# Kernel tuning notes

Hardware: AMD Instinct MI355X
Metric: run time of the kernel (lower is better)

## Reference

```python
import jax, jax.numpy as jnp
import numpy as np
import math

FACTOR = 5  # ProbAttention factor; scale=None -> 1/sqrt(D); mask_flag=True; output_attention=False


def setup_inputs() -> dict:
    key = jax.random.key(0)
    k1, k2, k3, k4 = jax.random.split(key, 4)
    B, L, H, D = 4, 2048, 8, 64
    sample_k = FACTOR * int(np.ceil(np.log(L)))  # 40
    queries = jax.random.normal(k1, (B, L, H, D), dtype=jnp.float32)
    keys = jax.random.normal(k2, (B, L, H, D), dtype=jnp.float32)
    values = jax.random.normal(k3, (B, L, H, D), dtype=jnp.float32)
    index_sample = jax.random.randint(k4, (L, sample_k), 0, L, dtype=jnp.int32)
    attn_mask = jnp.zeros((1,), dtype=bool)  # unused: ProbMask is rebuilt internally
    return {"queries": queries, "keys": keys, "values": values,
            "index_sample": index_sample, "attn_mask": attn_mask}


def reference(queries, keys, values, index_sample, attn_mask):
    B, L_Q, H, D = queries.shape
    L_K = keys.shape[1]
    # [B, L, H, D] -> [B, H, L, D]
    Q = jnp.transpose(queries, (0, 2, 1, 3))
    K = jnp.transpose(keys, (0, 2, 1, 3))
    V = jnp.transpose(values, (0, 2, 1, 3))

    U_part = max(1, min(FACTOR * int(math.ceil(math.log(L_K))), L_K))  # sample_k
    u = max(1, min(FACTOR * int(math.ceil(math.log(L_Q))), L_Q))       # n_top
    sample_k = U_part  # == index_sample.shape[1]

    # --- _prob_QK: sampled scores -> sparsity measure M -> top-u queries ---
    K_sample = K[:, :, index_sample, :]                       # [B,H,L_Q,sample_k,D]
    Q_K_sample = jnp.einsum('bhqd,bhqsd->bhqs', Q, K_sample)  # [B,H,L_Q,sample_k]
    M = Q_K_sample.max(axis=-1) - Q_K_sample.sum(axis=-1) / sample_k
    M_top = jax.lax.top_k(M, u)[1]                            # [B,H,u]

    Q_reduce = jnp.take_along_axis(Q, M_top[..., None], axis=2)   # [B,H,u,D]
    scale = 1.0 / math.sqrt(D)
    scores = jnp.einsum('bhud,bhkd->bhuk', Q_reduce, K) * scale   # [B,H,u,L_K]

    # --- initial context (mask_flag=True, L_Q == L_V): cumulative sum of V ---
    context = jnp.cumsum(V, axis=2)                               # [B,H,L_Q,D]

    # --- ProbMask: causal mask rows gathered at selected query positions ---
    causal = jnp.triu(jnp.ones((L_Q, L_K), dtype=bool), 1)
    mask = causal[M_top]                                          # [B,H,u,L_K]
    scores = jnp.where(mask, -jnp.inf, scores)

    attn = jax.nn.softmax(scores, axis=-1)
    upd = jnp.einsum('bhuk,bhkd->bhud', attn, V)                  # [B,H,u,D]

    b_idx = jnp.arange(B)[:, None, None]
    h_idx = jnp.arange(H)[None, :, None]
    context = context.at[b_idx, h_idx, M_top].set(upd)

    return jnp.transpose(context, (0, 2, 1, 3))  # [B,L_Q,H,D]
```

## Files before the change

kernel.cpp:

```cpp
#include <hip/hip_runtime.h>
#include <hip/hip_bf16.h>
#include <hip/hip_fp16.h>
#include <cstdint>

#define BB 4
#define LL 2048
#define HH 8
#define DD 64
#define SK 40
#define UU 40
#define LDK 68
#define NSEG32 64
#define NSEG64 32
#define PSTRIDE 34

__global__ __launch_bounds__(256) void k_sample_score(
    const float* __restrict__ Q, const float* __restrict__ K,
    const int* __restrict__ idxs, float* __restrict__ M) {
  int j = blockIdx.x;
  int xcd = j & 7, r = j >> 3;
  int bh = (xcd << 2) | (r >> 6);
  int qc = r & 63;
  int b = bh >> 3, h = bh & 7;
  int t = threadIdx.x;
  int ql = t >> 3, sp = t & 7;
  int q = qc * 32 + ql;

  __shared__ int sidx[SK][32];
  for (int i = t; i < SK * 32; i += 256)
    sidx[i >> 5][i & 31] = idxs[(qc * 32 + (i & 31)) * SK + (i >> 5)];
  __syncthreads();

  const float* qrow = Q + ((size_t)((b * LL + q) * HH + h)) * DD;
  float4 qa = *reinterpret_cast<const float4*>(qrow + sp * 4);
  float4 qb = *reinterpret_cast<const float4*>(qrow + 32 + sp * 4);

  const float* kb = K + (size_t)b * (LL * HH * DD) + h * DD;
  float mx = -1e30f, sm = 0.f;
#pragma unroll 4
  for (int s = 0; s < SK; s++) {
    int ks = sidx[s][ql];
    const float* kr = kb + (size_t)ks * (HH * DD);
    float4 ca = *reinterpret_cast<const float4*>(kr + sp * 4);
    float4 cb = *reinterpret_cast<const float4*>(kr + 32 + sp * 4);
    float dot = qa.x * ca.x + qa.y * ca.y + qa.z * ca.z + qa.w * ca.w +
                qb.x * cb.x + qb.y * cb.y + qb.z * cb.z + qb.w * cb.w;
    dot += __shfl_xor(dot, 1);
    dot += __shfl_xor(dot, 2);
    dot += __shfl_xor(dot, 4);
    mx = fmaxf(mx, dot);
    sm += dot;
  }
  if (sp == 0) M[bh * LL + q] = mx - sm * (1.0f / SK);
}

__global__ __launch_bounds__(256) void k_topk(const float* __restrict__ M,
                                              int* __restrict__ Mtop) {
  int bh = blockIdx.x;
  int t = threadIdx.x;
  __shared__ unsigned long long sk[LL];
  for (int i = t; i < LL; i += 256) {
    unsigned u = __float_as_uint(M[bh * LL + i]);
    u = (u & 0x80000000u) ? ~u : (u | 0x80000000u);
    sk[i] = ((unsigned long long)u << 32) | (unsigned)(~i);
  }
  __syncthreads();
  for (int k = 2; k <= LL; k <<= 1) {
    for (int j = k >> 1; j > 0; j >>= 1) {
#pragma unroll
      for (int m = 0; m < LL / 512; m++) {
        int p = t + m * 256;
        int i = ((p & ~(j - 1)) << 1) | (p & (j - 1));
        int l = i | j;
        unsigned long long a = sk[i], c = sk[l];
        bool asc = (i & k) == 0;
        if ((a > c) == asc) { sk[i] = c; sk[l] = a; }
      }
      __syncthreads();
    }
  }
  if (t < UU) {
    int e = (int)(~(unsigned)sk[LL - 1 - t]) & (LL - 1);
    Mtop[bh * UU + t] = e;
  }
}

__global__ __launch_bounds__(64) void k_chunksum16(const float* __restrict__ V,
                                                   float* __restrict__ CS16) {
  int j = blockIdx.x;
  int xcd = j & 7, r = j >> 3;
  int bh = (xcd << 2) | (r >> 7);
  int c = r & 127;
  int b = bh >> 3, h = bh & 7;
  int t = threadIdx.x, d4 = t & 15, r4 = t >> 4;
  const float4* vp = reinterpret_cast<const float4*>(
      V + ((size_t)((b * LL + c * 16 + r4 * 4) * HH + h)) * DD) + d4;
  float4 v0 = vp[0], v1 = vp[128], v2 = vp[256], v3 = vp[384];
  float4 s;
  s.x = v0.x + v1.x + v2.x + v3.x;
  s.y = v0.y + v1.y + v2.y + v3.y;
  s.z = v0.z + v1.z + v2.z + v3.z;
  s.w = v0.w + v1.w + v2.w + v3.w;
#pragma unroll
  for (int sh = 16; sh < 64; sh <<= 1) {
    s.x += __shfl_xor(s.x, sh);
    s.y += __shfl_xor(s.y, sh);
    s.z += __shfl_xor(s.z, sh);
    s.w += __shfl_xor(s.w, sh);
  }
  if (r4 == 0)
    *reinterpret_cast<float4*>(CS16 + ((size_t)bh * 128 + c) * 64 + d4 * 4) = s;
}

__global__ __launch_bounds__(256) void k_prefix16(const float* __restrict__ CS16,
                                                  float* __restrict__ PS16) {
  int bh = blockIdx.x;
  int t = threadIdx.x, w = t >> 6, d = t & 63;
  float cs[32];
  const float* base = CS16 + ((size_t)bh * 128 + w * 32) * 64 + d;
#pragma unroll
  for (int cc = 0; cc < 32; cc++) cs[cc] = base[cc * 64];
  float tot = 0.f;
#pragma unroll
  for (int cc = 0; cc < 32; cc++) tot += cs[cc];
  __shared__ float totw[4][64];
  totw[w][d] = tot;
  __syncthreads();
  float run = 0.f;
#pragma unroll
  for (int w2 = 0; w2 < 4; w2++)
    if (w2 < w) run += totw[w2][d];
  float* pbase = PS16 + ((size_t)bh * 128 + w * 32) * 64 + d;
#pragma unroll
  for (int cc = 0; cc < 32; cc++) { pbase[cc * 64] = run; run += cs[cc]; }
}

__global__ __launch_bounds__(64) void k_cumsum16(const float* __restrict__ V,
                                                 const float* __restrict__ PS16,
                                                 float* __restrict__ Out) {
  int j = blockIdx.x;
  int xcd = j & 7, r = j >> 3;
  int bh = (xcd << 2) | (r >> 7);
  int c = r & 127;
  int b = bh >> 3, h = bh & 7;
  int t = threadIdx.x, d4 = t & 15, r4 = t >> 4;
  size_t rowbase = ((size_t)((b * LL + c * 16 + r4 * 4) * HH + h)) * DD;
  const float4* vp = reinterpret_cast<const float4*>(V + rowbase) + d4;
  float4 v0 = vp[0], v1 = vp[128], v2 = vp[256], v3 = vp[384];
  float4 i0 = v0;
  float4 i1 = {i0.x + v1.x, i0.y + v1.y, i0.z + v1.z, i0.w + v1.w};
  float4 i2 = {i1.x + v2.x, i1.y + v2.y, i1.z + v2.z, i1.w + v2.w};
  float4 i3 = {i2.x + v3.x, i2.y + v3.y, i2.z + v3.z, i2.w + v3.w};
  float4 incl = i3;
  float4 u1;
  u1.x = __shfl_up(incl.x, 16); u1.y = __shfl_up(incl.y, 16);
  u1.z = __shfl_up(incl.z, 16); u1.w = __shfl_up(incl.w, 16);
  if (r4 >= 1) { incl.x += u1.x; incl.y += u1.y; incl.z += u1.z; incl.w += u1.w; }
  float4 u2;
  u2.x = __shfl_up(incl.x, 32); u2.y = __shfl_up(incl.y, 32);
  u2.z = __shfl_up(incl.z, 32); u2.w = __shfl_up(incl.w, 32);
  if (r4 >= 2) { incl.x += u2.x; incl.y += u2.y; incl.z += u2.z; incl.w += u2.w; }
  float4 ex = {incl.x - i3.x, incl.y - i3.y, incl.z - i3.z, incl.w - i3.w};
  float4 ps = *reinterpret_cast<const float4*>(
      PS16 + ((size_t)bh * 128 + c) * 64 + d4 * 4);
  float4 base4 = {ps.x + ex.x, ps.y + ex.y, ps.z + ex.z, ps.w + ex.w};
  float4* op = reinterpret_cast<float4*>(Out + rowbase) + d4;
  float4 o;
  o = {base4.x + i0.x, base4.y + i0.y, base4.z + i0.z, base4.w + i0.w}; op[0]   = o;
  o = {base4.x + i1.x, base4.y + i1.y, base4.z + i1.z, base4.w + i1.w}; op[128] = o;
  o = {base4.x + i2.x, base4.y + i2.y, base4.z + i2.z, base4.w + i2.w}; op[256] = o;
  o = {base4.x + i3.x, base4.y + i3.y, base4.z + i3.z, base4.w + i3.w}; op[384] = o;
}

__global__ __launch_bounds__(256) void k_attn_part32(
    const float* __restrict__ Q, const float* __restrict__ K,
    const float* __restrict__ V, const int* __restrict__ Mtop,
    float* __restrict__ Part) {
  int j = blockIdx.x;
  int xcd = j & 7, r_ = j >> 3;
  int bh = (xcd << 2) | (r_ & 3);
  int seg = r_ >> 2;
  int b = bh >> 3, h = bh & 7;
  int s0 = seg * 32;

  int t = threadIdx.x;
  int w = t >> 6, lane = t & 63;
  int kk = lane & 15, gg = lane >> 4;

  __shared__ float Kt[32 * LDK];
  __shared__ float psh[4][32];
  __shared__ int midx[UU];

  if (t < UU) midx[t] = Mtop[bh * UU + t];

  const float4* kg = reinterpret_cast<const float4*>(
      K + ((size_t)((b * LL + s0) * HH + h)) * DD);
#pragma unroll
  for (int i = 0; i < 2; i++) {
    int f = t + i * 256;
    int r = f >> 4, col = f & 15;
    float4 kv4 = kg[(size_t)r * (HH * DD / 4) + col];
    *reinterpret_cast<float4*>(&Kt[r * LDK + col * 4]) = kv4;
  }

  const float* vgp = V + ((size_t)((b * LL + s0) * HH + h)) * DD + lane;
  float vreg[32];
#pragma unroll
  for (int k = 0; k < 32; k++) vreg[k] = vgp[(size_t)k * (HH * DD)];

  __syncthreads();

  for (int uu = 0; uu < 10; uu++) {
    int u = w + uu * 4;
    int idx = midx[u];
    if (idx < s0) continue;
    int kend = idx - s0;
    if (kend > 31) kend = 31;

    const float4* qv = reinterpret_cast<const float4*>(
        Q + ((size_t)((b * LL + idx) * HH + h)) * DD + gg * 16);
    float4 qr0 = qv[0], qr1 = qv[1], qr2 = qv[2], qr3 = qv[3];

    float s0v, s1v;
    {
      const float4* kr = reinterpret_cast<const float4*>(&Kt[kk * LDK + gg * 16]);
      float4 c0 = kr[0], c1 = kr[1], c2 = kr[2], c3 = kr[3];
      float dp = qr0.x * c0.x + qr0.y * c0.y + qr0.z * c0.z + qr0.w * c0.w +
                 qr1.x * c1.x + qr1.y * c1.y + qr1.z * c1.z + qr1.w * c1.w +
                 qr2.x * c2.x + qr2.y * c2.y + qr2.z * c2.z + qr2.w * c2.w +
                 qr3.x * c3.x + qr3.y * c3.y + qr3.z * c3.z + qr3.w * c3.w;
      dp += __shfl_xor(dp, 16);
      dp += __shfl_xor(dp, 32);
      s0v = (kk <= kend) ? dp * 0.125f : -1e30f;
    }
    {
      const float4* kr = reinterpret_cast<const float4*>(&Kt[(16 + kk) * LDK + gg * 16]);
      float4 c0 = kr[0], c1 = kr[1], c2 = kr[2], c3 = kr[3];
      float dp = qr0.x * c0.x + qr0.y * c0.y + qr0.z * c0.z + qr0.w * c0.w +
                 qr1.x * c1.x + qr1.y * c1.y + qr1.z * c1.z + qr1.w * c1.w +
                 qr2.x * c2.x + qr2.y * c2.y + qr2.z * c2.z + qr2.w * c2.w +
                 qr3.x * c3.x + qr3.y * c3.y + qr3.z * c3.z + qr3.w * c3.w;
      dp += __shfl_xor(dp, 16);
      dp += __shfl_xor(dp, 32);
      s1v = (16 + kk <= kend) ? dp * 0.125f : -1e30f;
    }

    float m = fmaxf(s0v, s1v);
    m = fmaxf(m, __shfl_xor(m, 1));
    m = fmaxf(m, __shfl_xor(m, 2));
    m = fmaxf(m, __shfl_xor(m, 4));
    m = fmaxf(m, __shfl_xor(m, 8));
    float p0 = (kk <= kend) ? __expf(s0v - m) : 0.f;
    float p1 = (16 + kk <= kend) ? __expf(s1v - m) : 0.f;
    float l = p0 + p1;
    l += __shfl_xor(l, 1);
    l += __shfl_xor(l, 2);
    l += __shfl_xor(l, 4);
    l += __shfl_xor(l, 8);

    if (gg == 0) { psh[w][kk] = p0; psh[w][16 + kk] = p1; }

    float acc = 0.f;
#pragma unroll
    for (int kq = 0; kq < 8; kq++) {
      float4 pp = *reinterpret_cast<const float4*>(&psh[w][kq * 4]);
      acc += pp.x * vreg[kq * 4 + 0] + pp.y * vreg[kq * 4 + 1] +
             pp.z * vreg[kq * 4 + 2] + pp.w * vreg[kq * 4 + 3];
    }

    float* pb = Part + ((size_t)(bh * UU + u) * NSEG32 + seg) * PSTRIDE;
    __half* ph = reinterpret_cast<__half*>(pb + 2);
    ph[lane] = __float2half(acc);
    if (lane == 0) { pb[0] = m; pb[1] = l; }
  }
}

__global__ __launch_bounds__(256) void k_attn_part64(
    const float* __restrict__ Q, const float* __restrict__ K,
    const float* __restrict__ V, const int* __restrict__ Mtop,
    float* __restrict__ Part) {
  int j = blockIdx.x;
  int xcd = j & 7, r_ = j >> 3;
  int bh = (xcd << 2) | (r_ & 3);
  int seg = r_ >> 2;
  int b = bh >> 3, h = bh & 7;
  int s0 = seg * 64;

  int t = threadIdx.x;
  int w = t >> 6, lane = t & 63;
  int kk = lane & 15, gg = lane >> 4;

  __shared__ float Kt[64 * LDK];
  __shared__ float Vt[64 * LDK];
  __shared__ int midx[UU];

  if (t < UU) midx[t] = Mtop[bh * UU + t];

  const float4* kg = reinterpret_cast<const float4*>(
      K + ((size_t)((b * LL + s0) * HH + h)) * DD);
  const float4* vg = reinterpret_cast<const float4*>(
      V + ((size_t)((b * LL + s0) * HH + h)) * DD);
#pragma unroll
  for (int i = 0; i < 4; i++) {
    int f = t + i * 256;
    int r = f >> 4, col = f & 15;
    float4 kv4 = kg[(size_t)r * (HH * DD / 4) + col];
    float4 vv4 = vg[(size_t)r * (HH * DD / 4) + col];
    *reinterpret_cast<float4*>(&Kt[r * LDK + col * 4]) = kv4;
    *reinterpret_cast<float4*>(&Vt[r * LDK + col * 4]) = vv4;
  }
  __syncthreads();

  for (int uu = 0; uu < 10; uu++) {
    int u = w + uu * 4;
    int idx = midx[u];
    if (idx < s0) continue;
    int kend = idx - s0;
    if (kend > 63) kend = 63;

    const float4* qv = reinterpret_cast<const float4*>(
        Q + ((size_t)((b * LL + idx) * HH + h)) * DD + gg * 16);
    float4 qr0 = qv[0], qr1 = qv[1], qr2 = qv[2], qr3 = qv[3];

    float m = -1e30f, l = 0.f, acc = 0.f;
#pragma unroll
    for (int ks = 0; ks < 4; ks++) {
      if (ks * 16 > kend) break;
      int row = ks * 16 + kk;
      float dp = 0.f;
      const float4* kr = reinterpret_cast<const float4*>(&Kt[row * LDK + gg * 16]);
      float4 c0 = kr[0], c1 = kr[1], c2 = kr[2], c3 = kr[3];
      dp += qr0.x * c0.x + qr0.y * c0.y + qr0.z * c0.z + qr0.w * c0.w;
      dp += qr1.x * c1.x + qr1.y * c1.y + qr1.z * c1.z + qr1.w * c1.w;
      dp += qr2.x * c2.x + qr2.y * c2.y + qr2.z * c2.z + qr2.w * c2.w;
      dp += qr3.x * c3.x + qr3.y * c3.y + qr3.z * c3.z + qr3.w * c3.w;
      dp += __shfl_xor(dp, 16);
      dp += __shfl_xor(dp, 32);
      bool valid = (row <= kend);
      float s = valid ? dp * 0.125f : -1e30f;
      float cm = s;
      cm = fmaxf(cm, __shfl_xor(cm, 1));
      cm = fmaxf(cm, __shfl_xor(cm, 2));
      cm = fmaxf(cm, __shfl_xor(cm, 4));
      cm = fmaxf(cm, __shfl_xor(cm, 8));
      float mn = fmaxf(m, cm);
      float f_ = __expf(m - mn);
      float p = valid ? __expf(s - mn) : 0.f;
      float ps = p;
      ps += __shfl_xor(ps, 1);
      ps += __shfl_xor(ps, 2);
      ps += __shfl_xor(ps, 4);
      ps += __shfl_xor(ps, 8);
      l = l * f_ + ps;
      m = mn;
      acc *= f_;
#pragma unroll
      for (int k2 = 0; k2 < 16; k2++) {
        float pk = __shfl(p, k2);
        acc += pk * Vt[(ks * 16 + k2) * LDK + lane];
      }
    }

    float* pb = Part + ((size_t)(bh * UU + u) * NSEG64 + seg) * PSTRIDE;
    __half* ph = reinterpret_cast<__half*>(pb + 2);
    ph[lane] = __float2half(acc);
    if (lane == 0) { pb[0] = m; pb[1] = l; }
  }
}

__global__ __launch_bounds__(64) void k_attn_merge(
    const int* __restrict__ Mtop, const float* __restrict__ Part,
    float* __restrict__ Out, int shift, int nsegmax) {
  int blk = blockIdx.x;
  int bh = blk / UU, u = blk % UU;
  int b = bh >> 3, h = bh & 7;
  int lane = threadIdx.x;
  int idx = Mtop[bh * UU + u];
  int nseg = (idx >> shift) + 1;

  const float* base = Part + (size_t)(bh * UU + u) * nsegmax * PSTRIDE;
  float ms = -1e30f, ls = 0.f;
  if (lane < nseg) { ms = base[lane * PSTRIDE]; ls = base[lane * PSTRIDE + 1]; }
  float M0 = ms;
#pragma unroll
  for (int s = 1; s < 64; s <<= 1) M0 = fmaxf(M0, __shfl_xor(M0, s));
  float e = (lane < nseg) ? __expf(ms - M0) : 0.f;
  float lt = ls * e;
#pragma unroll
  for (int s = 1; s < 64; s <<= 1) lt += __shfl_xor(lt, s);

  __shared__ float ew[64];
  ew[lane] = e;
  __syncthreads();

  float A = 0.f;
  for (int s = 0; s < nseg; s++) {
    const __half* ha = reinterpret_cast<const __half*>(base + s * PSTRIDE + 2);
    A += ew[s] * __half2float(ha[lane]);
  }
  Out[((size_t)((b * LL + idx) * HH + h)) * DD + lane] = A / lt;
}

__global__ __launch_bounds__(256) void k_attn_fused(
    const float* __restrict__ Q, const float* __restrict__ K,
    const float* __restrict__ V, const int* __restrict__ Mtop,
    float* __restrict__ Out) {
  int j = blockIdx.x;
  int xcd = j & 7, slot = j >> 3;
  int bh = (xcd << 2) | (slot / 40);
  int u = slot % 40;
  int b = bh >> 3, h = bh & 7;
  int idx = Mtop[bh * UU + u];

  int t = threadIdx.x;
  int w = t >> 6, lane = t & 63;
  int kk = lane & 15, gg = lane >> 4;

  __shared__ float Kt[64 * LDK];
  __shared__ float Vt[64 * LDK];
  __shared__ float qs[64];

  const float* qp = Q + ((size_t)((b * LL + idx) * HH + h)) * DD;
  if (t < 64) qs[t] = qp[t] * 0.125f;
  __syncthreads();

  float qr[16];
#pragma unroll
  for (int jj = 0; jj < 16; jj++) qr[jj] = qs[gg * 16 + jj];

  float m = -1e30f, l = 0.f, acc = 0.f;
  int nch = (idx + 64) >> 6;

  for (int ch = 0; ch < nch; ch++) {
    __syncthreads();
    const float4* kg = reinterpret_cast<const float4*>(K + ((size_t)((b * LL + ch * 64) * HH + h)) * DD);
    const float4* vg = reinterpret_cast<const float4*>(V + ((size_t)((b * LL + ch * 64) * HH + h)) * DD);
#pragma unroll
    for (int i = 0; i < 4; i++) {
      int f = t + i * 256;
      int r = f >> 4, col = f & 15;
      float4 kv4 = kg[(size_t)r * (HH * DD / 4) + col];
      float4 vv4 = vg[(size_t)r * (HH * DD / 4) + col];
      *reinterpret_cast<float4*>(&Kt[r * LDK + col * 4]) = kv4;
      *reinterpret_cast<float4*>(&Vt[r * LDK + col * 4]) = vv4;
    }
    __syncthreads();

    int row = w * 16 + kk;
    int key = ch * 64 + row;
    float dp = 0.f;
#pragma unroll
    for (int jj = 0; jj < 4; jj++) {
      float4 kv4 = *reinterpret_cast<const float4*>(&Kt[row * LDK + gg * 16 + jj * 4]);
      dp += qr[jj * 4 + 0] * kv4.x + qr[jj * 4 + 1] * kv4.y +
            qr[jj * 4 + 2] * kv4.z + qr[jj * 4 + 3] * kv4.w;
    }
    dp += __shfl_xor(dp, 16);
    dp += __shfl_xor(dp, 32);
    bool valid = (key <= idx);
    float s = valid ? dp : -1e30f;
    float cm = s;
    cm = fmaxf(cm, __shfl_xor(cm, 1));
    cm = fmaxf(cm, __shfl_xor(cm, 2));
    cm = fmaxf(cm, __shfl_xor(cm, 4));
    cm = fmaxf(cm, __shfl_xor(cm, 8));
    float mn = fmaxf(m, cm);
    float f_ = __expf(m - mn);
    float p = valid ? __expf(s - mn) : 0.f;
    float ps = p;
    ps += __shfl_xor(ps, 1);
    ps += __shfl_xor(ps, 2);
    ps += __shfl_xor(ps, 4);
    ps += __shfl_xor(ps, 8);
    l = l * f_ + ps;
    m = mn;
    acc *= f_;
#pragma unroll
    for (int k2 = 0; k2 < 16; k2++) {
      float pk = __shfl(p, k2);
      acc += pk * Vt[(w * 16 + k2) * LDK + lane];
    }
  }

  __syncthreads();
  float* mw = Kt;
  float* lw = Kt + 8;
  float* aw = Vt;
  if (lane == 0) { mw[w] = m; lw[w] = l; }
  aw[w * 64 + lane] = acc;
  __syncthreads();
  if (w == 0) {
    float M0 = fmaxf(fmaxf(mw[0], mw[1]), fmaxf(mw[2], mw[3]));
    float Lt = 0.f, A = 0.f;
#pragma unroll
    for (int i = 0; i < 4; i++) {
      float e = __expf(mw[i] - M0);
      Lt += lw[i] * e;
      A += aw[i * 64 + lane] * e;
    }
    Out[((size_t)((b * LL + idx) * HH + h)) * DD + lane] = A / Lt;
  }
}

extern "C" void kernel_launch(void* const* d_in, const int* in_sizes, int n_in,
                              void* d_out, int out_size, void* d_ws, size_t ws_size,
                              hipStream_t stream) {
  const float* Q = (const float*)d_in[0];
  const float* K = (const float*)d_in[1];
  const float* V = (const float*)d_in[2];
  const int* IS = (const int*)d_in[3];
  float* Out = (float*)d_out;

  float* M = (float*)d_ws;
  float* CS16 = M + BB * HH * LL;
  float* PS16 = CS16 + BB * HH * 128 * DD;
  int* Mtop = (int*)(PS16 + BB * HH * 128 * DD);
  float* Part = (float*)(Mtop + BB * HH * UU);
  size_t fixed = (size_t)(BB * HH * LL + 2 * BB * HH * 128 * DD) * 4 +
                 (size_t)(BB * HH * UU) * 4;
  size_t need32 = fixed + (size_t)(BB * HH * UU) * NSEG32 * PSTRIDE * 4;
  size_t need64 = fixed + (size_t)(BB * HH * UU) * NSEG64 * PSTRIDE * 4;

  k_sample_score<<<2048, 256, 0, stream>>>(Q, K, IS, M);
  k_topk<<<BB * HH, 256, 0, stream>>>(M, Mtop);
  k_chunksum16<<<4096, 64, 0, stream>>>(V, CS16);
  k_prefix16<<<BB * HH, 256, 0, stream>>>(CS16, PS16);
  k_cumsum16<<<4096, 64, 0, stream>>>(V, PS16, Out);
  if (ws_size >= need32) {
    k_attn_part32<<<2048, 256, 0, stream>>>(Q, K, V, Mtop, Part);
    k_attn_merge<<<BB * HH * UU, 64, 0, stream>>>(Mtop, Part, Out, 5, NSEG32);
  } else if (ws_size >= need64) {
    k_attn_part64<<<1024, 256, 0, stream>>>(Q, K, V, Mtop, Part);
    k_attn_merge<<<BB * HH * UU, 64, 0, stream>>>(Mtop, Part, Out, 6, NSEG64);
  } else {
    k_attn_fused<<<BB * HH * UU, 256, 0, stream>>>(Q, K, V, Mtop, Out);
  }
}
```

Baseline: 181.4 us.

## Replace bitonic sort top-k with radix-select threshold search

```diff
diff --git a/kernel.cpp b/kernel.cpp
--- a/kernel.cpp
+++ b/kernel.cpp
@@ -58,30 +58,88 @@
                                               int* __restrict__ Mtop) {
   int bh = blockIdx.x;
   int t = threadIdx.x;
-  __shared__ unsigned long long sk[LL];
-  for (int i = t; i < LL; i += 256) {
-    unsigned u = __float_as_uint(M[bh * LL + i]);
-    u = (u & 0x80000000u) ? ~u : (u | 0x80000000u);
-    sk[i] = ((unsigned long long)u << 32) | (unsigned)(~i);
-  }
-  __syncthreads();
-  for (int k = 2; k <= LL; k <<= 1) {
-    for (int j = k >> 1; j > 0; j >>= 1) {
-#pragma unroll
-      for (int m = 0; m < LL / 512; m++) {
-        int p = t + m * 256;
-        int i = ((p & ~(j - 1)) << 1) | (p & (j - 1));
-        int l = i | j;
-        unsigned long long a = sk[i], c = sk[l];
-        bool asc = (i & k) == 0;
-        if ((a > c) == asc) { sk[i] = c; sk[l] = a; }
+  __shared__ int hist[256];
+  __shared__ int eqbuf[LL];
+  __shared__ int selcnt, eqcnt, T_s, gt_s;
+
+  unsigned vals[8];
+#pragma unroll
+  for (int i = 0; i < 8; i++) {
+    unsigned u = __float_as_uint(M[bh * LL + i * 256 + t]);
+    vals[i] = (u & 0x80000000u) ? ~u : (u | 0x80000000u);
+  }
+
+  unsigned prefix = 0;
+  int rem = UU;
+  for (int lvl = 0; lvl < 4; lvl++) {
+    int sh = 24 - 8 * lvl;
+    hist[t] = 0;
+    if (t == 0) { T_s = 0; gt_s = 0; }
+    __syncthreads();
+#pragma unroll
+    for (int i = 0; i < 8; i++) {
+      unsigned v = vals[i];
+      bool act = (((unsigned long long)v >> (sh + 8)) == (unsigned long long)prefix);
+      if (act) atomicAdd(&hist[(v >> sh) & 255], 1);
+    }
+    __syncthreads();
+    if (t < 64) {
+      int h0 = hist[t * 4], h1 = hist[t * 4 + 1];
+      int h2 = hist[t * 4 + 2], h3 = hist[t * 4 + 3];
+      int gs = h0 + h1 + h2 + h3;
+      int acc = gs;
+#pragma unroll
+      for (int off = 1; off < 64; off <<= 1) {
+        int x = __shfl_down(acc, off);
+        if (t + off < 64) acc += x;
       }
-      __syncthreads();
-    }
-  }
-  if (t < UU) {
-    int e = (int)(~(unsigned)sk[LL - 1 - t]) & (LL - 1);
-    Mtop[bh * UU + t] = e;
+      int sufGT = acc - gs;
+      int s3 = h3 + sufGT;
+      int s2 = h2 + s3;
+      int s1 = h1 + s2;
+      int s0 = h0 + s1;
+      if (s0 > rem && s1 <= rem)    { T_s = t * 4 + 0; gt_s = s1; }
+      if (s1 > rem && s2 <= rem)    { T_s = t * 4 + 1; gt_s = s2; }
+      if (s2 > rem && s3 <= rem)    { T_s = t * 4 + 2; gt_s = s3; }
+      if (s3 > rem && sufGT <= rem) { T_s = t * 4 + 3; gt_s = sufGT; }
+    }
+    __syncthreads();
+    prefix = (prefix << 8) | (unsigned)T_s;
+    rem -= gt_s;
+    __syncthreads();
+  }
+  unsigned tv = prefix;
+
+  if (t == 0) { selcnt = 0; eqcnt = 0; }
+  __syncthreads();
+#pragma unroll
+  for (int i = 0; i < 8; i++) {
+    unsigned v = vals[i];
+    int idx = i * 256 + t;
+    if (v > tv) {
+      int p = atomicAdd(&selcnt, 1);
+      Mtop[bh * UU + p] = idx;
+    } else if (v == tv) {
+      int p = atomicAdd(&eqcnt, 1);
+      eqbuf[p] = idx;
+    }
+  }
+  __syncthreads();
+  int base = selcnt;
+  int needEq = UU - base;
+  int E = eqcnt;
+  if (needEq > 0) {
+    if (E == needEq) {
+      for (int e = t; e < E; e += 256)
+        Mtop[bh * UU + base + e] = eqbuf[e];
+    } else {
+      for (int e = t; e < E; e += 256) {
+        int my = eqbuf[e];
+        int rnk = 0;
+        for (int f = 0; f < E; f++) rnk += (eqbuf[f] < my);
+        if (rnk < needEq) Mtop[bh * UU + base + rnk] = my;
+      }
+    }
   }
 }
 
```

Result: faster. 160.0 us (-11.8%).
